# Optimization experiments

Measured on AMD Instinct MI355X. Metric: run time of the kernel, lower is better.

The kernel has to match this reference:

```python
import jax, jax.numpy as jnp
import numpy as np

N = 10000
E = 160000
NT = 4      # num_types
NB = 8      # bessel basis size
U = 32      # env_embed_multiplicity
R_MAX = 6.0
AVG_NEIGH = 16.0
POLY_P = 6.0


def _mlp(x, Ws):
    # nequip ScalarMLPFunction: no biases, forward-normalized weights, SiLU between layers
    n = len(Ws)
    for i, W in enumerate(Ws):
        x = x @ (W * (1.0 / jnp.sqrt(jnp.float32(W.shape[0]))))
        if i < n - 1:
            x = jax.nn.silu(x)
    return x


def _poly_cutoff(r, rc, p=POLY_P):
    x = r / rc
    out = (1.0 - ((p + 1.0) * (p + 2.0) / 2.0) * x ** p
           + p * (p + 2.0) * x ** (p + 1.0)
           - (p * (p + 1.0) / 2.0) * x ** (p + 2.0))
    return out * (x < 1.0)


def _weighted_channels(edge_attr, w):
    # MakeWeightedChannels: per-edge, per-channel weight for each irrep block
    # edge_attr: [E,4] = (0e | 1o), w: [E,U,2] -> out [E,U,4]
    wd = jnp.concatenate([w[:, :, 0:1], jnp.repeat(w[:, :, 1:2], 3, axis=-1)], axis=-1)
    return edge_attr[:, None, :] * wd


def _forward(edge_index, node_attrs, edge_attr, edge_embed, edge_length,
             W2b0, W2b1, W2b2, Wenv0, Wlat0, Wlat1, Wenv1, Wfin0, Wfin1,
             Wlin_s, Wlin_v, resnet_params):
    n_nodes = node_attrs.shape[0]
    n_edges = edge_attr.shape[0]
    center, neigh = edge_index[0], edge_index[1]
    cut = _poly_cutoff(edge_length, R_MAX)[:, None]           # [E,1], same per-layer cutoff
    env_norm = 1.0 / jnp.sqrt(AVG_NEIGH)
    sqrt3 = jnp.sqrt(3.0)
    c = jnp.exp(resnet_params)                                 # resnet update coefficients

    # ---- two-body latent (layer 0 latent)
    lat_in = jnp.concatenate([node_attrs[center], node_attrs[neigh], edge_embed], axis=-1)
    latents = _mlp(lat_in, [W2b0, W2b1, W2b2]) * cut           # [E,512]
    norm2 = c[0] ** 2
    latents = latents * (c[0] / jnp.sqrt(norm2))

    # env-embed MLP layer 0: feature weights + env weights
    w0 = _mlp(latents, [Wenv0])                                # [E,4U]
    w_feat = w0[:, :2 * U].reshape(n_edges, U, 2)
    w_env = w0[:, 2 * U:].reshape(n_edges, U, 2)
    features = _weighted_channels(edge_attr, w_feat)           # [E,U,4]

    def env_embed_edges(w_env):
        env_w = _weighted_channels(edge_attr, w_env)           # [E,U,4]
        env = jax.ops.segment_sum(env_w, center, num_segments=n_nodes) * env_norm
        return env[center]                                     # [E,U,4]

    # ---- layer 0 TP ('uuu', e3nn component norm): (0e+1o) x (0e+1o) -> [0e,0e,1o,1o]
    env_e = env_embed_edges(w_env)
    t0 = features[:, :, 0] * env_e[:, :, 0]
    t1 = jnp.sum(features[:, :, 1:] * env_e[:, :, 1:], axis=-1) / sqrt3
    v0 = features[:, :, 0:1] * env_e[:, :, 1:]
    v1 = features[:, :, 1:] * env_e[:, :, 0:1]
    scalars = jnp.concatenate([t0, t1], axis=-1)               # [E,2U]
    # e3nn Linear mixing full_out_irreps back to (0e+1o) x U
    alpha = 1.0 / jnp.sqrt(2.0 * U)
    y_s = (scalars @ Wlin_s) * alpha                           # [E,U]
    x_v = jnp.concatenate([v0, v1], axis=1)                    # [E,2U,3]
    y_v = jnp.einsum('ekd,ko->eod', x_v, Wlin_v) * alpha       # [E,U,3]
    features = jnp.concatenate([y_s[..., None], y_v], axis=-1)

    # latent resnet update
    new_lat = _mlp(jnp.concatenate([latents, scalars], axis=-1), [Wlat0, Wlat1]) * cut
    latents = (jnp.sqrt(norm2) * latents + c[1] * new_lat) / jnp.sqrt(norm2 + c[1] ** 2)
    norm2 = norm2 + c[1] ** 2

    w_env = _mlp(latents, [Wenv1]).reshape(n_edges, U, 2)

    # ---- layer 1 TP (last layer): only scalar outputs [0e,0e]
    env_e = env_embed_edges(w_env)
    t0 = features[:, :, 0] * env_e[:, :, 0]
    t1 = jnp.sum(features[:, :, 1:] * env_e[:, :, 1:], axis=-1) / sqrt3
    scalars = jnp.concatenate([t0, t1], axis=-1)               # [E,2U]
    # (the last-layer Linear output features are never used downstream -> skipped)

    # ---- final latent
    new_lat = _mlp(jnp.concatenate([latents, scalars], axis=-1), [Wfin0, Wfin1]) * cut
    latents = (jnp.sqrt(norm2) * latents + c[2] * new_lat) / jnp.sqrt(norm2 + c[2] ** 2)
    return latents                                             # [E,512] edge features


def setup_inputs() -> dict:
    key = jax.random.key(0)
    ks = jax.random.split(key, 20)
    edge_index = jax.random.randint(ks[0], (2, E), 0, N)
    node_types = jax.random.randint(ks[1], (N,), 0, NT)
    node_attrs = jax.nn.one_hot(node_types, NT, dtype=jnp.float32)
    edge_length = jax.random.uniform(ks[2], (E,), minval=0.5, maxval=R_MAX)
    vec = jax.random.normal(ks[3], (E, 3), dtype=jnp.float32)
    unit = vec / jnp.linalg.norm(vec, axis=-1, keepdims=True)
    # component-normalized real spherical harmonics: l=0 -> 1, l=1 -> sqrt(3)*unit
    edge_attr = jnp.concatenate([jnp.ones((E, 1), jnp.float32), jnp.sqrt(3.0) * unit], axis=-1)
    nb = jnp.arange(1, NB + 1, dtype=jnp.float32)
    edge_embed = (jnp.sqrt(2.0 / R_MAX)
                  * jnp.sin(nb[None, :] * jnp.pi * edge_length[:, None] / R_MAX)
                  / edge_length[:, None])
    w = lambda k, shp: jax.random.normal(k, shp, dtype=jnp.float32)
    return {
        'edge_index': edge_index, 'node_attrs': node_attrs, 'edge_attr': edge_attr,
        'edge_embed': edge_embed, 'edge_length': edge_length,
        'W2b0': w(ks[4], (2 * NT + NB, 128)), 'W2b1': w(ks[5], (128, 256)), 'W2b2': w(ks[6], (256, 512)),
        'Wenv0': w(ks[7], (512, 4 * U)),
        'Wlat0': w(ks[8], (512 + 2 * U, 512)), 'Wlat1': w(ks[9], (512, 512)),
        'Wenv1': w(ks[10], (512, 2 * U)),
        'Wfin0': w(ks[11], (512 + 2 * U, 512)), 'Wfin1': w(ks[12], (512, 512)),
        'Wlin_s': w(ks[13], (2 * U, U)), 'Wlin_v': w(ks[14], (2 * U, U)),
        'resnet_params': jnp.zeros((3,), jnp.float32),
    }


def reference(edge_index, node_attrs, edge_attr, edge_embed, edge_length,
              W2b0, W2b1, W2b2, Wenv0, Wlat0, Wlat1, Wenv1, Wfin0, Wfin1,
              Wlin_s, Wlin_v, resnet_params):
    return _forward(edge_index, node_attrs, edge_attr, edge_embed, edge_length,
                    W2b0, W2b1, W2b2, Wenv0, Wlat0, Wlat1, Wenv1, Wfin0, Wfin1,
                    Wlin_s, Wlin_v, resnet_params)
```

## Files before the change

kernel.cpp:

```cpp
#include <hip/hip_runtime.h>
#include <math.h>

#define E_EDGES 160000
#define N_NODES 10000

typedef __attribute__((ext_vector_type(8))) __bf16 bf16x8;
typedef __attribute__((ext_vector_type(4))) float f32x4;
typedef __attribute__((ext_vector_type(4))) unsigned int u32x4;

__device__ __forceinline__ unsigned short f2bf(float x) {
    unsigned u = __float_as_uint(x);
    u += 0x7fff + ((u >> 16) & 1);
    return (unsigned short)(u >> 16);
}
__device__ __forceinline__ float bf2f(unsigned short h) {
    return __uint_as_float(((unsigned)h) << 16);
}
__device__ __forceinline__ float siluf(float v) {
    return v / (1.0f + __expf(-v));
}
__device__ __forceinline__ void gload16(const unsigned short* g, unsigned short* l) {
    __builtin_amdgcn_global_load_lds(
        (const __attribute__((address_space(1))) void*)g,
        (__attribute__((address_space(3))) void*)l, 16, 0, 0);
}

__global__ __launch_bounds__(256)
void prep_kernel(const int* __restrict__ ei, const float* __restrict__ na,
                 const float* __restrict__ embed, const float* __restrict__ elen,
                 float* __restrict__ cut, unsigned short* __restrict__ A16b,
                 int* __restrict__ deg)
{
    int e = blockIdx.x * blockDim.x + threadIdx.x;
    if (e >= E_EDGES) return;
    float r  = elen[e];
    float x  = r * (1.0f / 6.0f);
    float x2 = x * x;
    float x6 = x2 * x2 * x2;
    float c = 1.0f - 28.0f * x6 + 48.0f * x6 * x - 21.0f * x6 * x2;
    cut[e] = (x < 1.0f) ? c : 0.0f;
    int ctr = ei[e];
    int ngh = ei[E_EDGES + e];
    atomicAdd(&deg[ctr], 1);
    float4 ac = *(const float4*)(na + (size_t)ctr * 4);
    float4 an = *(const float4*)(na + (size_t)ngh * 4);
    float4 b0 = *(const float4*)(embed + (size_t)e * 8);
    float4 b1 = *(const float4*)(embed + (size_t)e * 8 + 4);
    unsigned short* o = A16b + (size_t)e * 32;
    o[0]  = f2bf(ac.x); o[1]  = f2bf(ac.y); o[2]  = f2bf(ac.z); o[3]  = f2bf(ac.w);
    o[4]  = f2bf(an.x); o[5]  = f2bf(an.y); o[6]  = f2bf(an.z); o[7]  = f2bf(an.w);
    o[8]  = f2bf(b0.x); o[9]  = f2bf(b0.y); o[10] = f2bf(b0.z); o[11] = f2bf(b0.w);
    o[12] = f2bf(b1.x); o[13] = f2bf(b1.y); o[14] = f2bf(b1.z); o[15] = f2bf(b1.w);
    #pragma unroll
    for (int i = 16; i < 32; ++i) o[i] = 0;
}

__global__ __launch_bounds__(256)
void wtrans_all(const float* __restrict__ w0, const float* __restrict__ w1,
                const float* __restrict__ w2, const float* __restrict__ w3,
                const float* __restrict__ w4, const float* __restrict__ w5,
                const float* __restrict__ w6, const float* __restrict__ w7,
                const float* __restrict__ w8, unsigned short* __restrict__ wbuf)
{
    int blk = blockIdx.x;
    const float* W; int K, N, Kpad, Npad; size_t dbase; int lstart; float sc;
    const float s16  = 0.25f;
    const float s128 = 0.088388347648318447f;
    const float s256 = 0.0625f;
    const float s512 = 0.044194173824159223f;
    const float s576 = 0.041666666666666664f;
    if      (blk <   16) { W=w0; K=16;  N=128; Kpad=32;  Npad=128; dbase=0;       lstart=0;    sc=s16;  }
    else if (blk <  144) { W=w1; K=128; N=256; Kpad=128; Npad=256; dbase=4096;    lstart=16;   sc=s128; }
    else if (blk <  656) { W=w2; K=256; N=512; Kpad=256; Npad=512; dbase=36864;   lstart=144;  sc=s256; }
    else if (blk <  912) { W=w3; K=512; N=128; Kpad=512; Npad=128; dbase=167936;  lstart=656;  sc=s512; }
    else if (blk < 2064) { W=w4; K=576; N=512; Kpad=576; Npad=512; dbase=233472;  lstart=912;  sc=s576; }
    else if (blk < 3088) { W=w5; K=512; N=512; Kpad=512; Npad=512; dbase=528384;  lstart=2064; sc=s512; }
    else if (blk < 3344) { W=w6; K=512; N=64;  Kpad=512; Npad=128; dbase=790528;  lstart=3088; sc=s512; }
    else if (blk < 4496) { W=w7; K=576; N=512; Kpad=576; Npad=512; dbase=856064;  lstart=3344; sc=s576; }
    else                 { W=w8; K=512; N=512; Kpad=512; Npad=512; dbase=1150976; lstart=4496; sc=s512; }
    int local = (blk - lstart) * 256 + threadIdx.x;
    int n = local % Npad, k = local / Npad;
    if (k >= Kpad) return;
    float v = (k < K && n < N) ? W[(size_t)k * N + n] * sc : 0.0f;
    wbuf[dbase + (size_t)n * Kpad + k] = f2bf(v);
}

__global__ __launch_bounds__(1024)
void scan_kernel(const int* __restrict__ deg, int* __restrict__ offs)
{
    __shared__ int part[1024];
    int t = threadIdx.x;
    int base = t * 10;
    int loc[10];
    int s = 0;
    #pragma unroll
    for (int i = 0; i < 10; ++i) {
        int idx = base + i;
        int d = (idx < N_NODES) ? deg[idx] : 0;
        loc[i] = s; s += d;
    }
    part[t] = s;
    __syncthreads();
    for (int o = 1; o < 1024; o <<= 1) {
        int v = (t >= o) ? part[t - o] : 0;
        __syncthreads();
        part[t] += v;
        __syncthreads();
    }
    int excl = (t > 0) ? part[t - 1] : 0;
    #pragma unroll
    for (int i = 0; i < 10; ++i) {
        int idx = base + i;
        if (idx < N_NODES) offs[idx] = excl + loc[i];
    }
    if (t == 1023) offs[N_NODES] = part[1023];
}

__global__ __launch_bounds__(256)
void fill_kernel(const int* __restrict__ ei, const int* __restrict__ offs,
                 int* __restrict__ cnt, int* __restrict__ elist)
{
    int e = blockIdx.x * blockDim.x + threadIdx.x;
    if (e >= E_EDGES) return;
    int c = ei[e];
    int pos = offs[c] + atomicAdd(&cnt[c], 1);
    elist[pos] = e;
}

__global__ __launch_bounds__(256)
void sortseg_kernel(const int* __restrict__ offs, int* __restrict__ elist)
{
    int node = blockIdx.x * 4 + (threadIdx.x >> 6);
    int l = threadIdx.x & 63;
    if (node >= N_NODES) return;
    int b = offs[node], en = offs[node + 1];
    int deg = en - b;
    if (deg <= 1) return;
    if (deg <= 64) {
        int v = (l < deg) ? elist[b + l] : 0x7fffffff;
        #pragma unroll
        for (int k = 2; k <= 64; k <<= 1) {
            #pragma unroll
            for (int j = k >> 1; j > 0; j >>= 1) {
                int o = __shfl_xor(v, j);
                bool dirUp = ((l & k) == 0);
                bool lower = ((l & j) == 0);
                int mn = v < o ? v : o;
                int mx = v < o ? o : v;
                v = (dirUp == lower) ? mn : mx;
            }
        }
        if (l < deg) elist[b + l] = v;
    } else if (l == 0) {
        for (int i = b + 1; i < en; ++i) {
            int v = elist[i];
            int j = i - 1;
            while (j >= b && elist[j] > v) { elist[j + 1] = elist[j]; --j; }
            elist[j + 1] = v;
        }
    }
}

__global__ __launch_bounds__(256)
void envgather_kernel(const unsigned short* __restrict__ Wb, int wstride, int woff,
                      const float* __restrict__ ea, const int* __restrict__ offs,
                      const int* __restrict__ elist, float* __restrict__ env)
{
    int n = blockIdx.x * 2 + (threadIdx.x >> 7);
    int t = threadIdx.x & 127;
    if (n >= N_NODES) return;
    int u = t >> 2, comp = t & 3;
    int widx = woff + u * 2 + (comp ? 1 : 0);
    int beg = offs[n], end = offs[n + 1];
    float acc = 0.0f;
    for (int i = beg; i < end; ++i) {
        int e = elist[i];
        float w = bf2f(Wb[(size_t)e * wstride + widx]);
        float a = ea[(size_t)e * 4 + comp];
        acc += a * w;
    }
    env[(size_t)n * 128 + t] = acc * 0.25f;
}

__global__ __launch_bounds__(512)
void mlp2b(const unsigned short* __restrict__ A16b,
           const unsigned short* __restrict__ W0t,
           const unsigned short* __restrict__ W1t,
           const unsigned short* __restrict__ W2t,
           const unsigned short* __restrict__ Wet,
           const float* __restrict__ cut,
           unsigned short* __restrict__ Lb,
           unsigned short* __restrict__ R1b)
{
    __shared__ __align__(16) unsigned short SA[64 * 32];
    __shared__ __align__(16) unsigned short RG[64 * 512];
    unsigned short* H1 = RG;
    unsigned short* H2 = RG + 8192;
    const int tid  = threadIdx.x;
    const int lane = tid & 63;
    const int wid  = tid >> 6;
    const int l15  = lane & 15;
    const int l4r  = lane >> 2;
    const int lk8  = (lane >> 4) << 3;
    const int sk8  = (((lane & 3) ^ ((lane >> 3) & 3)) << 3);
    const int rk8  = ((((lane >> 4) ^ ((l15 >> 1) & 3)) & 3) << 3);
    const int bm   = blockIdx.x * 64;
    const int hrow4 = (lane >> 4) << 2;

    if (wid < 4) {
        int row = (wid << 4) + l4r;
        gload16(A16b + (size_t)(bm + row) * 32 + sk8, &SA[wid << 9]);
    }
    asm volatile("s_waitcnt vmcnt(0)" ::: "memory");
    __builtin_amdgcn_s_barrier();
    __builtin_amdgcn_sched_barrier(0);

    {
        int hc = wid * 16 + l15;
        bf16x8 wf = __builtin_bit_cast(bf16x8, *(const u32x4*)(W0t + (size_t)hc * 32 + lk8));
        #pragma unroll
        for (int mi = 0; mi < 4; ++mi) {
            bf16x8 af = __builtin_bit_cast(bf16x8, *(const u32x4*)&SA[(mi * 16 + l15) * 32 + rk8]);
            f32x4 a = {};
            a = __builtin_amdgcn_mfma_f32_16x16x32_bf16(af, wf, a, 0, 0, 0);
            #pragma unroll
            for (int rr = 0; rr < 4; ++rr) {
                int er = mi * 16 + hrow4 + rr;
                H1[er * 128 + (((hc >> 3) ^ (er & 7)) << 3) + (hc & 7)] = f2bf(siluf(a[rr]));
            }
        }
    }
    asm volatile("s_waitcnt lgkmcnt(0)" ::: "memory");
    __builtin_amdgcn_s_barrier();
    __builtin_amdgcn_sched_barrier(0);

    {
        f32x4 acc[4][2] = {};
        #pragma unroll
        for (int kt = 0; kt < 4; ++kt) {
            bf16x8 hf[4], wf[2];
            #pragma unroll
            for (int fa = 0; fa < 4; ++fa) {
                int er = fa * 16 + l15;
                int slotp = (kt * 4 + (lane >> 4)) ^ (er & 7);
                hf[fa] = __builtin_bit_cast(bf16x8, *(const u32x4*)&H1[er * 128 + slotp * 8]);
            }
            #pragma unroll
            for (int fb = 0; fb < 2; ++fb) {
                int hc = wid * 32 + fb * 16 + l15;
                wf[fb] = __builtin_bit_cast(bf16x8, *(const u32x4*)(W1t + (size_t)hc * 128 + kt * 32 + lk8));
            }
            #pragma unroll
            for (int fa = 0; fa < 4; ++fa)
                #pragma unroll
                for (int fb = 0; fb < 2; ++fb)
                    acc[fa][fb] = __builtin_amdgcn_mfma_f32_16x16x32_bf16(hf[fa], wf[fb], acc[fa][fb], 0, 0, 0);
        }
        asm volatile("s_waitcnt lgkmcnt(0)" ::: "memory");
        __builtin_amdgcn_s_barrier();
        #pragma unroll
        for (int fa = 0; fa < 4; ++fa)
            #pragma unroll
            for (int fb = 0; fb < 2; ++fb)
                #pragma unroll
                for (int rr = 0; rr < 4; ++rr) {
                    int er = fa * 16 + hrow4 + rr;
                    int hc = wid * 32 + fb * 16 + l15;
                    H2[er * 256 + (((hc >> 3) ^ (er & 7)) << 3) + (hc & 7)] = f2bf(siluf(acc[fa][fb][rr]));
                }
    }
    asm volatile("s_waitcnt lgkmcnt(0)" ::: "memory");
    __builtin_amdgcn_s_barrier();
    __builtin_amdgcn_sched_barrier(0);

    f32x4 acc[4][4] = {};
    #pragma unroll 1
    for (int kt = 0; kt < 8; ++kt) {
        bf16x8 hf[4], wf[4];
        #pragma unroll
        for (int fa = 0; fa < 4; ++fa) {
            int er = fa * 16 + l15;
            int slotp = (kt * 4 + (lane >> 4)) ^ (er & 7);
            hf[fa] = __builtin_bit_cast(bf16x8, *(const u32x4*)&H2[er * 256 + slotp * 8]);
        }
        #pragma unroll
        for (int fb = 0; fb < 4; ++fb) {
            int oc = wid * 64 + fb * 16 + l15;
            wf[fb] = __builtin_bit_cast(bf16x8, *(const u32x4*)(W2t + (size_t)oc * 256 + kt * 32 + lk8));
        }
        __builtin_amdgcn_s_setprio(1);
        #pragma unroll
        for (int fa = 0; fa < 4; ++fa)
            #pragma unroll
            for (int fb = 0; fb < 4; ++fb)
                acc[fa][fb] = __builtin_amdgcn_mfma_f32_16x16x32_bf16(hf[fa], wf[fb], acc[fa][fb], 0, 0, 0);
        __builtin_amdgcn_s_setprio(0);
    }
    asm volatile("s_waitcnt lgkmcnt(0)" ::: "memory");
    __builtin_amdgcn_s_barrier();
    __builtin_amdgcn_sched_barrier(0);

    #pragma unroll
    for (int fa = 0; fa < 4; ++fa) {
        int rbase = bm + fa * 16 + hrow4;
        #pragma unroll
        for (int fb = 0; fb < 4; ++fb) {
            int col = wid * 64 + fb * 16 + l15;
            #pragma unroll
            for (int rr = 0; rr < 4; ++rr) {
                int row = rbase + rr;
                int er  = fa * 16 + hrow4 + rr;
                float v = acc[fa][fb][rr] * cut[row];
                unsigned short b = f2bf(v);
                Lb[(size_t)row * 512 + col] = b;
                RG[er * 512 + (((col >> 3) ^ (er & 7)) << 3) + (col & 7)] = b;
            }
        }
    }
    asm volatile("s_waitcnt lgkmcnt(0)" ::: "memory");
    __builtin_amdgcn_s_barrier();
    __builtin_amdgcn_sched_barrier(0);

    {
        f32x4 acce[4] = {};
        int oc = wid * 16 + l15;
        #pragma unroll 1
        for (int kt = 0; kt < 16; ++kt) {
            bf16x8 wfe = __builtin_bit_cast(bf16x8, *(const u32x4*)(Wet + (size_t)oc * 512 + kt * 32 + lk8));
            #pragma unroll
            for (int fa = 0; fa < 4; ++fa) {
                int er = fa * 16 + l15;
                int slotp = (kt * 4 + (lane >> 4)) ^ (er & 7);
                bf16x8 afe = __builtin_bit_cast(bf16x8, *(const u32x4*)&RG[er * 512 + slotp * 8]);
                acce[fa] = __builtin_amdgcn_mfma_f32_16x16x32_bf16(afe, wfe, acce[fa], 0, 0, 0);
            }
        }
        #pragma unroll
        for (int fa = 0; fa < 4; ++fa) {
            int rbase = bm + fa * 16 + hrow4;
            #pragma unroll
            for (int rr = 0; rr < 4; ++rr)
                R1b[(size_t)(rbase + rr) * 128 + wid * 16 + l15] = f2bf(acce[fa][rr]);
        }
    }
}

template<int EPIL2, bool ENV>
__global__ __launch_bounds__(512)
void fused_mlp(const unsigned short* __restrict__ A1,
               const unsigned short* __restrict__ A2,
               const unsigned short* __restrict__ W1t,
               const unsigned short* __restrict__ W2t,
               const unsigned short* __restrict__ Wet,
               float* __restrict__ Cf, unsigned short* __restrict__ Cb,
               unsigned short* __restrict__ Weo,
               const float* __restrict__ cut, const float* __restrict__ rp)
{
    __shared__ __align__(16) unsigned short Hl[128 * 512];
    __shared__ __align__(16) unsigned short SA[3][128 * 32];
    const int tid  = threadIdx.x;
    const int lane = tid & 63;
    const int wid  = tid >> 6;
    const int l15  = lane & 15;
    const int l4r  = lane >> 2;
    const int lk8  = (lane >> 4) << 3;
    const int sk8  = (((lane & 3) ^ ((lane >> 3) & 3)) << 3);
    const int rk8  = ((((lane >> 4) ^ ((l15 >> 1) & 3)) & 3) << 3);
    const int bm   = blockIdx.x * 128;
    const int col0 = wid * 64;
    const int hrow4 = (lane >> 4) << 2;

    auto stage = [&](int t, int b) {
        int k0 = t << 5;
        int row = (wid << 4) + l4r;
        const unsigned short* gp;
        if (k0 < 512) gp = A1 + (size_t)(bm + row) * 512 + k0 + sk8;
        else          gp = A2 + (size_t)(bm + row) * 64 + (k0 - 512) + sk8;
        gload16(gp, &SA[b][wid << 9]);
    };

    f32x4 acc1[8][4] = {};
    stage(0, 0);
    stage(1, 1);

    for (int t = 0; t < 18; ++t) {
        __builtin_amdgcn_sched_barrier(0);
        if (t < 17) asm volatile("s_waitcnt vmcnt(1)" ::: "memory");
        else        asm volatile("s_waitcnt vmcnt(0)" ::: "memory");
        __builtin_amdgcn_s_barrier();
        __builtin_amdgcn_sched_barrier(0);

        const unsigned short* As = &SA[t % 3][0];
        int k0 = t << 5;
        bf16x8 af[8], wf[4];
        #pragma unroll
        for (int mi = 0; mi < 8; ++mi)
            af[mi] = __builtin_bit_cast(bf16x8, *(const u32x4*)&As[(mi * 16 + l15) * 32 + rk8]);
        #pragma unroll
        for (int ni = 0; ni < 4; ++ni) {
            int hc = col0 + ni * 16 + l15;
            wf[ni] = __builtin_bit_cast(bf16x8, *(const u32x4*)(W1t + (size_t)hc * 576 + k0 + lk8));
        }
        __builtin_amdgcn_sched_barrier(0);
        if (t + 2 < 18) stage(t + 2, (t + 2) % 3);
        __builtin_amdgcn_sched_barrier(0);
        asm volatile("s_waitcnt lgkmcnt(0)" ::: "memory");
        __builtin_amdgcn_sched_barrier(0);

        __builtin_amdgcn_s_setprio(1);
        #pragma unroll
        for (int mi = 0; mi < 8; ++mi)
            #pragma unroll
            for (int ni = 0; ni < 4; ++ni)
                acc1[mi][ni] = __builtin_amdgcn_mfma_f32_16x16x32_bf16(af[mi], wf[ni], acc1[mi][ni], 0, 0, 0);
        __builtin_amdgcn_s_setprio(0);
    }

    #pragma unroll
    for (int mi = 0; mi < 8; ++mi)
        #pragma unroll
        for (int ni = 0; ni < 4; ++ni)
            #pragma unroll
            for (int rr = 0; rr < 4; ++rr) {
                int er = mi * 16 + hrow4 + rr;
                int hc = col0 + ni * 16 + l15;
                Hl[er * 512 + (((hc >> 3) ^ (er & 7)) << 3) + (hc & 7)] = f2bf(siluf(acc1[mi][ni][rr]));
            }
    asm volatile("s_waitcnt lgkmcnt(0)" ::: "memory");
    __builtin_amdgcn_s_barrier();
    __builtin_amdgcn_sched_barrier(0);

    f32x4 acc2[8][4] = {};
    #pragma unroll 1
    for (int kt = 0; kt < 16; ++kt) {
        bf16x8 hf[8], w2f[4];
        #pragma unroll
        for (int fa = 0; fa < 8; ++fa) {
            int er = fa * 16 + l15;
            int slotp = (kt * 4 + (lane >> 4)) ^ (er & 7);
            hf[fa] = __builtin_bit_cast(bf16x8, *(const u32x4*)&Hl[er * 512 + slotp * 8]);
        }
        #pragma unroll
        for (int fb = 0; fb < 4; ++fb) {
            int oc = col0 + fb * 16 + l15;
            w2f[fb] = __builtin_bit_cast(bf16x8, *(const u32x4*)(W2t + (size_t)oc * 512 + kt * 32 + lk8));
        }
        __builtin_amdgcn_s_setprio(1);
        #pragma unroll
        for (int fa = 0; fa < 8; ++fa)
            #pragma unroll
            for (int fb = 0; fb < 4; ++fb)
                acc2[fa][fb] = __builtin_amdgcn_mfma_f32_16x16x32_bf16(hf[fa], w2f[fb], acc2[fa][fb], 0, 0, 0);
        __builtin_amdgcn_s_setprio(0);
    }

    if constexpr (ENV) {
        asm volatile("s_waitcnt lgkmcnt(0)" ::: "memory");
        __builtin_amdgcn_s_barrier();
        __builtin_amdgcn_sched_barrier(0);
    }

    float c0 = __expf(rp[0]), c1 = __expf(rp[1]), c2 = __expf(rp[2]);
    #pragma unroll
    for (int fa = 0; fa < 8; ++fa) {
        int rbase = bm + fa * 16 + hrow4;
        #pragma unroll
        for (int fb = 0; fb < 4; ++fb) {
            int col = col0 + fb * 16 + l15;
            #pragma unroll
            for (int rr = 0; rr < 4; ++rr) {
                int row = rbase + rr;
                int er  = fa * 16 + hrow4 + rr;
                float v = acc2[fa][fb][rr];
                size_t off2 = (size_t)row * 512 + col;
                if (EPIL2 == 3) {
                    float old = bf2f(Cb[off2]);
                    v = (c0 * old + c1 * v * cut[row]) * rsqrtf(c0 * c0 + c1 * c1);
                    unsigned short b = f2bf(v);
                    Cb[off2] = b;
                    if constexpr (ENV)
                        Hl[er * 512 + (((col >> 3) ^ (er & 7)) << 3) + (col & 7)] = b;
                } else {
                    float old = bf2f(Cb[off2]);
                    float n2 = c0 * c0 + c1 * c1;
                    v = (sqrtf(n2) * old + c2 * v * cut[row]) * rsqrtf(n2 + c2 * c2);
                    Cf[off2] = v;
                }
            }
        }
    }

    if constexpr (ENV) {
        asm volatile("s_waitcnt lgkmcnt(0)" ::: "memory");
        __builtin_amdgcn_s_barrier();
        __builtin_amdgcn_sched_barrier(0);
        f32x4 acce[4] = {};
        int er = wid * 16 + l15;
        #pragma unroll 1
        for (int kt = 0; kt < 16; ++kt) {
            int slotp = (kt * 4 + (lane >> 4)) ^ (er & 7);
            bf16x8 afe = __builtin_bit_cast(bf16x8, *(const u32x4*)&Hl[er * 512 + slotp * 8]);
            #pragma unroll
            for (int fb = 0; fb < 4; ++fb) {
                int oc = fb * 16 + l15;
                bf16x8 wfe = __builtin_bit_cast(bf16x8, *(const u32x4*)(Wet + (size_t)oc * 512 + kt * 32 + lk8));
                acce[fb] = __builtin_amdgcn_mfma_f32_16x16x32_bf16(afe, wfe, acce[fb], 0, 0, 0);
            }
        }
        #pragma unroll
        for (int fb = 0; fb < 4; ++fb) {
            int col = fb * 16 + l15;
            #pragma unroll
            for (int rr = 0; rr < 4; ++rr) {
                int row = bm + wid * 16 + hrow4 + rr;
                Weo[(size_t)row * 64 + col] = f2bf(acce[fb][rr]);
            }
        }
    }
}

__global__ __launch_bounds__(256)
void tp0_kernel(const unsigned short* __restrict__ W0b, const float* __restrict__ ea,
                const float* __restrict__ env, const int* __restrict__ ei,
                const float* __restrict__ Ws, const float* __restrict__ Wv,
                unsigned short* __restrict__ scalb, unsigned short* __restrict__ feat2b)
{
    __shared__ float sc[8][64];
    __shared__ float xv[8][64][3];
    __shared__ float Wsl[2048];
    __shared__ float Wvl[2048];
    int tid = threadIdx.x;
    const float alpha = 0.125f;
    #pragma unroll
    for (int i = 0; i < 8; ++i) {
        Wsl[tid + i * 256] = Ws[tid + i * 256] * alpha;
        Wvl[tid + i * 256] = Wv[tid + i * 256] * alpha;
    }
    int le = tid >> 5;
    int u  = tid & 31;
    int e  = blockIdx.x * 8 + le;
    int c  = ei[e];
    float4 a = *(const float4*)(ea + (size_t)e * 4);
    const float* ep = env + (size_t)c * 128 + u * 4;
    float e0 = ep[0], e1 = ep[1], e2 = ep[2], e3 = ep[3];
    float wf0 = bf2f(W0b[(size_t)e * 128 + u * 2]);
    float wf1 = bf2f(W0b[(size_t)e * 128 + u * 2 + 1]);
    float f0 = a.x * wf0;
    float f1 = a.y * wf1, f2 = a.z * wf1, f3 = a.w * wf1;
    const float rs3 = 0.57735026918962576f;
    float t0 = f0 * e0;
    float t1 = (f1 * e1 + f2 * e2 + f3 * e3) * rs3;
    scalb[(size_t)e * 64 + u]      = f2bf(t0);
    scalb[(size_t)e * 64 + 32 + u] = f2bf(t1);
    sc[le][u]      = t0;
    sc[le][32 + u] = t1;
    xv[le][u][0] = f0 * e1; xv[le][u][1] = f0 * e2; xv[le][u][2] = f0 * e3;
    xv[le][32 + u][0] = f1 * e0; xv[le][32 + u][1] = f2 * e0; xv[le][32 + u][2] = f3 * e0;
    __syncthreads();
    float ys = 0.0f, yv0 = 0.0f, yv1 = 0.0f, yv2 = 0.0f;
    #pragma unroll 8
    for (int k = 0; k < 64; ++k) {
        float ws = Wsl[k * 32 + u];
        float wv = Wvl[k * 32 + u];
        ys  = fmaf(sc[le][k], ws, ys);
        yv0 = fmaf(xv[le][k][0], wv, yv0);
        yv1 = fmaf(xv[le][k][1], wv, yv1);
        yv2 = fmaf(xv[le][k][2], wv, yv2);
    }
    ushort4 ov;
    ov.x = f2bf(ys);
    ov.y = f2bf(yv0);
    ov.z = f2bf(yv1);
    ov.w = f2bf(yv2);
    *(ushort4*)(feat2b + (size_t)e * 128 + u * 4) = ov;
}

__global__ __launch_bounds__(256)
void tp1_kernel(const unsigned short* __restrict__ feat2b, const float* __restrict__ env,
                const int* __restrict__ ei, unsigned short* __restrict__ scalb)
{
    int idx = blockIdx.x * blockDim.x + threadIdx.x;
    if (idx >= E_EDGES * 32) return;
    int e = idx >> 5, u = idx & 31;
    int c = ei[e];
    const float* ep = env + (size_t)c * 128 + u * 4;
    ushort4 f4 = *(const ushort4*)(feat2b + (size_t)e * 128 + u * 4);
    float fx = bf2f(f4.x), fy = bf2f(f4.y), fz = bf2f(f4.z), fw = bf2f(f4.w);
    const float rs3 = 0.57735026918962576f;
    float t0 = fx * ep[0];
    float t1 = (fy * ep[1] + fz * ep[2] + fw * ep[3]) * rs3;
    scalb[(size_t)e * 64 + u]      = f2bf(t0);
    scalb[(size_t)e * 64 + 32 + u] = f2bf(t1);
}

extern "C" void kernel_launch(void* const* d_in, const int* in_sizes, int n_in,
                              void* d_out, int out_size, void* d_ws, size_t ws_size,
                              hipStream_t stream)
{
    const int*   ei     = (const int*)d_in[0];
    const float* na     = (const float*)d_in[1];
    const float* ea     = (const float*)d_in[2];
    const float* embed  = (const float*)d_in[3];
    const float* elen   = (const float*)d_in[4];
    const float* W2b0   = (const float*)d_in[5];
    const float* W2b1   = (const float*)d_in[6];
    const float* W2b2   = (const float*)d_in[7];
    const float* Wenv0  = (const float*)d_in[8];
    const float* Wlat0  = (const float*)d_in[9];
    const float* Wlat1  = (const float*)d_in[10];
    const float* Wenv1  = (const float*)d_in[11];
    const float* Wfin0  = (const float*)d_in[12];
    const float* Wfin1  = (const float*)d_in[13];
    const float* Wlin_s = (const float*)d_in[14];
    const float* Wlin_v = (const float*)d_in[15];
    const float* rp     = (const float*)d_in[16];

    float* L = (float*)d_out;
    const size_t E = E_EDGES;

    char* ws = (char*)d_ws;
    size_t off = 0;
    auto alloc = [&](size_t b) { void* p = ws + off; off += (b + 255) & ~(size_t)255; return p; };
    float*          cutb   = (float*)alloc(E * 4);
    unsigned short* wbuf   = (unsigned short*)alloc((size_t)1413120 * 2);
    float*          envb   = (float*)alloc((size_t)N_NODES * 128 * 4);
    unsigned short* scalb  = (unsigned short*)alloc(E * 64 * 2);
    unsigned short* feat2b = (unsigned short*)alloc(E * 128 * 2);
    unsigned short* Lb     = (unsigned short*)alloc(E * 512 * 2);
    int*            degcnt = (int*)alloc((size_t)2 * N_NODES * 4);
    int*            offs   = (int*)alloc((N_NODES + 1) * 4);
    int*            elist  = (int*)alloc(E * 4);
    unsigned short* A16b   = (unsigned short*)alloc(E * 32 * 2);
    unsigned short* R1b    = (unsigned short*)alloc(E * 128 * 2);
    unsigned short* WE1b   = (unsigned short*)alloc(E * 64 * 2);
    int* deg = degcnt;
    int* cnt = degcnt + N_NODES;

    unsigned short* W2b0t  = wbuf;
    unsigned short* W2b1t  = wbuf + 4096;
    unsigned short* W2b2t  = wbuf + 36864;
    unsigned short* Wenv0t = wbuf + 167936;
    unsigned short* Wlat0t = wbuf + 233472;
    unsigned short* Wlat1t = wbuf + 528384;
    unsigned short* Wenv1t = wbuf + 790528;
    unsigned short* Wfin0t = wbuf + 856064;
    unsigned short* Wfin1t = wbuf + 1150976;
    wtrans_all<<<5520, 256, 0, stream>>>(W2b0, W2b1, W2b2, Wenv0, Wlat0, Wlat1,
                                         Wenv1, Wfin0, Wfin1, wbuf);

    hipMemsetAsync(degcnt, 0, (size_t)2 * N_NODES * 4, stream);
    prep_kernel<<<E_EDGES / 256, 256, 0, stream>>>(ei, na, embed, elen, cutb, A16b, deg);
    scan_kernel<<<1, 1024, 0, stream>>>(deg, offs);
    fill_kernel<<<E_EDGES / 256, 256, 0, stream>>>(ei, offs, cnt, elist);
    sortseg_kernel<<<N_NODES / 4, 256, 0, stream>>>(offs, elist);

    mlp2b<<<2500, 512, 0, stream>>>(A16b, W2b0t, W2b1t, W2b2t, Wenv0t, cutb, Lb, R1b);

    envgather_kernel<<<N_NODES / 2, 256, 0, stream>>>(R1b, 128, 64, ea, offs, elist, envb);
    tp0_kernel<<<E_EDGES / 8, 256, 0, stream>>>(R1b, ea, envb, ei, Wlin_s, Wlin_v, scalb, feat2b);

    fused_mlp<3, true><<<1250, 512, 0, stream>>>(Lb, scalb, Wlat0t, Wlat1t, Wenv1t,
                                                 nullptr, Lb, WE1b, cutb, rp);

    envgather_kernel<<<N_NODES / 2, 256, 0, stream>>>(WE1b, 64, 0, ea, offs, elist, envb);
    tp1_kernel<<<E_EDGES * 32 / 256, 256, 0, stream>>>(feat2b, envb, ei, scalb);

    fused_mlp<4, false><<<1250, 512, 0, stream>>>(Lb, scalb, Wfin0t, Wfin1t, nullptr,
                                                  L, Lb, nullptr, cutb, rp);
}
```

Measured before the change: 1.196 ms.

## Stage first-GEMM weight tiles into LDS via async loads in fused MLP kernels

The first GEMM in both fused MLP kernels used to read W1 fragments straight from global memory every k-step. It now streams the 512x32 weight tile into the otherwise idle Hl buffer with async global-to-LDS loads, triple-buffered next to the A tiles, and reads fragments from LDS. The template is split into two concrete kernels, waits are adjusted to vmcnt(5), and a barrier is added before Hl is reused for the hidden activations. This is meant to hide global weight-load latency behind the MFMA work, at the cost of more LDS traffic and more outstanding loads per wave.

```diff
diff --git a/kernel.cpp b/kernel.cpp
--- a/kernel.cpp
+++ b/kernel.cpp
@@ -345,16 +345,15 @@
     }
 }
 
-template<int EPIL2, bool ENV>
 __global__ __launch_bounds__(512)
-void fused_mlp(const unsigned short* __restrict__ A1,
-               const unsigned short* __restrict__ A2,
-               const unsigned short* __restrict__ W1t,
-               const unsigned short* __restrict__ W2t,
-               const unsigned short* __restrict__ Wet,
-               float* __restrict__ Cf, unsigned short* __restrict__ Cb,
-               unsigned short* __restrict__ Weo,
-               const float* __restrict__ cut, const float* __restrict__ rp)
+void fused_mlp3env(const unsigned short* __restrict__ A1,
+                   const unsigned short* __restrict__ A2,
+                   const unsigned short* __restrict__ W1t,
+                   const unsigned short* __restrict__ W2t,
+                   const unsigned short* __restrict__ Wet,
+                   unsigned short* __restrict__ Cb,
+                   unsigned short* __restrict__ Weo,
+                   const float* __restrict__ cut, const float* __restrict__ rp)
 {
     __shared__ __align__(16) unsigned short Hl[128 * 512];
     __shared__ __align__(16) unsigned short SA[3][128 * 32];
@@ -370,7 +369,7 @@
     const int col0 = wid * 64;
     const int hrow4 = (lane >> 4) << 2;
 
-    auto stage = [&](int t, int b) {
+    auto stageA = [&](int t, int b) {
         int k0 = t << 5;
         int row = (wid << 4) + l4r;
         const unsigned short* gp;
@@ -378,34 +377,37 @@
         else          gp = A2 + (size_t)(bm + row) * 64 + (k0 - 512) + sk8;
         gload16(gp, &SA[b][wid << 9]);
     };
+    auto stageW = [&](int t, int b) {
+        int k0 = t << 5;
+        #pragma unroll
+        for (int i = 0; i < 4; ++i) {
+            int ch  = (wid << 2) + i;
+            int row = (ch << 4) + l4r;
+            gload16(W1t + (size_t)row * 576 + k0 + sk8, &Hl[b * 16384 + (ch << 9)]);
+        }
+    };
 
     f32x4 acc1[8][4] = {};
-    stage(0, 0);
-    stage(1, 1);
+    stageA(0, 0); stageW(0, 0);
+    stageA(1, 1); stageW(1, 1);
 
     for (int t = 0; t < 18; ++t) {
-        __builtin_amdgcn_sched_barrier(0);
-        if (t < 17) asm volatile("s_waitcnt vmcnt(1)" ::: "memory");
+        if (t < 17) asm volatile("s_waitcnt vmcnt(5)" ::: "memory");
         else        asm volatile("s_waitcnt vmcnt(0)" ::: "memory");
         __builtin_amdgcn_s_barrier();
         __builtin_amdgcn_sched_barrier(0);
 
+        if (t + 2 < 18) { stageA(t + 2, (t + 2) % 3); stageW(t + 2, (t + 2) % 3); }
+
         const unsigned short* As = &SA[t % 3][0];
-        int k0 = t << 5;
+        const unsigned short* Ws = &Hl[(t % 3) * 16384];
         bf16x8 af[8], wf[4];
         #pragma unroll
         for (int mi = 0; mi < 8; ++mi)
             af[mi] = __builtin_bit_cast(bf16x8, *(const u32x4*)&As[(mi * 16 + l15) * 32 + rk8]);
         #pragma unroll
-        for (int ni = 0; ni < 4; ++ni) {
-            int hc = col0 + ni * 16 + l15;
-            wf[ni] = __builtin_bit_cast(bf16x8, *(const u32x4*)(W1t + (size_t)hc * 576 + k0 + lk8));
-        }
-        __builtin_amdgcn_sched_barrier(0);
-        if (t + 2 < 18) stage(t + 2, (t + 2) % 3);
-        __builtin_amdgcn_sched_barrier(0);
-        asm volatile("s_waitcnt lgkmcnt(0)" ::: "memory");
-        __builtin_amdgcn_sched_barrier(0);
+        for (int ni = 0; ni < 4; ++ni)
+            wf[ni] = __builtin_bit_cast(bf16x8, *(const u32x4*)&Ws[(col0 + ni * 16 + l15) * 32 + rk8]);
 
         __builtin_amdgcn_s_setprio(1);
         #pragma unroll
@@ -415,6 +417,9 @@
                 acc1[mi][ni] = __builtin_amdgcn_mfma_f32_16x16x32_bf16(af[mi], wf[ni], acc1[mi][ni], 0, 0, 0);
         __builtin_amdgcn_s_setprio(0);
     }
+    asm volatile("s_waitcnt lgkmcnt(0)" ::: "memory");
+    __builtin_amdgcn_s_barrier();
+    __builtin_amdgcn_sched_barrier(0);
 
     #pragma unroll
     for (int mi = 0; mi < 8; ++mi)
@@ -454,13 +459,11 @@
         __builtin_amdgcn_s_setprio(0);
     }
 
-    if constexpr (ENV) {
-        asm volatile("s_waitcnt lgkmcnt(0)" ::: "memory");
-        __builtin_amdgcn_s_barrier();
-        __builtin_amdgcn_sched_barrier(0);
-    }
-
-    float c0 = __expf(rp[0]), c1 = __expf(rp[1]), c2 = __expf(rp[2]);
+    asm volatile("s_waitcnt lgkmcnt(0)" ::: "memory");
+    __builtin_amdgcn_s_barrier();
+    __builtin_amdgcn_sched_barrier(0);
+
+    float c0 = __expf(rp[0]), c1 = __expf(rp[1]);
     #pragma unroll
     for (int fa = 0; fa < 8; ++fa) {
         int rbase = bm + fa * 16 + hrow4;
@@ -473,27 +476,19 @@
                 int er  = fa * 16 + hrow4 + rr;
                 float v = acc2[fa][fb][rr];
                 size_t off2 = (size_t)row * 512 + col;
-                if (EPIL2 == 3) {
-                    float old = bf2f(Cb[off2]);
-                    v = (c0 * old + c1 * v * cut[row]) * rsqrtf(c0 * c0 + c1 * c1);
-                    unsigned short b = f2bf(v);
-                    Cb[off2] = b;
-                    if constexpr (ENV)
-                        Hl[er * 512 + (((col >> 3) ^ (er & 7)) << 3) + (col & 7)] = b;
-                } else {
-                    float old = bf2f(Cb[off2]);
-                    float n2 = c0 * c0 + c1 * c1;
-                    v = (sqrtf(n2) * old + c2 * v * cut[row]) * rsqrtf(n2 + c2 * c2);
-                    Cf[off2] = v;
-                }
-            }
-        }
-    }
-
-    if constexpr (ENV) {
-        asm volatile("s_waitcnt lgkmcnt(0)" ::: "memory");
-        __builtin_amdgcn_s_barrier();
-        __builtin_amdgcn_sched_barrier(0);
+                float old = bf2f(Cb[off2]);
+                v = (c0 * old + c1 * v * cut[row]) * rsqrtf(c0 * c0 + c1 * c1);
+                unsigned short b = f2bf(v);
+                Cb[off2] = b;
+                Hl[er * 512 + (((col >> 3) ^ (er & 7)) << 3) + (col & 7)] = b;
+            }
+        }
+    }
+    asm volatile("s_waitcnt lgkmcnt(0)" ::: "memory");
+    __builtin_amdgcn_s_barrier();
+    __builtin_amdgcn_sched_barrier(0);
+
+    {
         f32x4 acce[4] = {};
         int er = wid * 16 + l15;
         #pragma unroll 1
@@ -514,6 +509,139 @@
             for (int rr = 0; rr < 4; ++rr) {
                 int row = bm + wid * 16 + hrow4 + rr;
                 Weo[(size_t)row * 64 + col] = f2bf(acce[fb][rr]);
+            }
+        }
+    }
+}
+
+__global__ __launch_bounds__(512)
+void fused_mlp4(const unsigned short* __restrict__ A1,
+                const unsigned short* __restrict__ A2,
+                const unsigned short* __restrict__ W1t,
+                const unsigned short* __restrict__ W2t,
+                float* __restrict__ Cf, const unsigned short* __restrict__ Cb,
+                const float* __restrict__ cut, const float* __restrict__ rp)
+{
+    __shared__ __align__(16) unsigned short Hl[128 * 512];
+    __shared__ __align__(16) unsigned short SA[3][128 * 32];
+    const int tid  = threadIdx.x;
+    const int lane = tid & 63;
+    const int wid  = tid >> 6;
+    const int l15  = lane & 15;
+    const int l4r  = lane >> 2;
+    const int lk8  = (lane >> 4) << 3;
+    const int sk8  = (((lane & 3) ^ ((lane >> 3) & 3)) << 3);
+    const int rk8  = ((((lane >> 4) ^ ((l15 >> 1) & 3)) & 3) << 3);
+    const int bm   = blockIdx.x * 128;
+    const int col0 = wid * 64;
+    const int hrow4 = (lane >> 4) << 2;
+
+    auto stageA = [&](int t, int b) {
+        int k0 = t << 5;
+        int row = (wid << 4) + l4r;
+        const unsigned short* gp;
+        if (k0 < 512) gp = A1 + (size_t)(bm + row) * 512 + k0 + sk8;
+        else          gp = A2 + (size_t)(bm + row) * 64 + (k0 - 512) + sk8;
+        gload16(gp, &SA[b][wid << 9]);
+    };
+    auto stageW = [&](int t, int b) {
+        int k0 = t << 5;
+        #pragma unroll
+        for (int i = 0; i < 4; ++i) {
+            int ch  = (wid << 2) + i;
+            int row = (ch << 4) + l4r;
+            gload16(W1t + (size_t)row * 576 + k0 + sk8, &Hl[b * 16384 + (ch << 9)]);
+        }
+    };
+
+    f32x4 acc1[8][4] = {};
+    stageA(0, 0); stageW(0, 0);
+    stageA(1, 1); stageW(1, 1);
+
+    for (int t = 0; t < 18; ++t) {
+        if (t < 17) asm volatile("s_waitcnt vmcnt(5)" ::: "memory");
+        else        asm volatile("s_waitcnt vmcnt(0)" ::: "memory");
+        __builtin_amdgcn_s_barrier();
+        __builtin_amdgcn_sched_barrier(0);
+
+        if (t + 2 < 18) { stageA(t + 2, (t + 2) % 3); stageW(t + 2, (t + 2) % 3); }
+
+        const unsigned short* As = &SA[t % 3][0];
+        const unsigned short* Ws = &Hl[(t % 3) * 16384];
+        bf16x8 af[8], wf[4];
+        #pragma unroll
+        for (int mi = 0; mi < 8; ++mi)
+            af[mi] = __builtin_bit_cast(bf16x8, *(const u32x4*)&As[(mi * 16 + l15) * 32 + rk8]);
+        #pragma unroll
+        for (int ni = 0; ni < 4; ++ni)
+            wf[ni] = __builtin_bit_cast(bf16x8, *(const u32x4*)&Ws[(col0 + ni * 16 + l15) * 32 + rk8]);
+
+        __builtin_amdgcn_s_setprio(1);
+        #pragma unroll
+        for (int mi = 0; mi < 8; ++mi)
+            #pragma unroll
+            for (int ni = 0; ni < 4; ++ni)
+                acc1[mi][ni] = __builtin_amdgcn_mfma_f32_16x16x32_bf16(af[mi], wf[ni], acc1[mi][ni], 0, 0, 0);
+        __builtin_amdgcn_s_setprio(0);
+    }
+    asm volatile("s_waitcnt lgkmcnt(0)" ::: "memory");
+    __builtin_amdgcn_s_barrier();
+    __builtin_amdgcn_sched_barrier(0);
+
+    #pragma unroll
+    for (int mi = 0; mi < 8; ++mi)
+        #pragma unroll
+        for (int ni = 0; ni < 4; ++ni)
+            #pragma unroll
+            for (int rr = 0; rr < 4; ++rr) {
+                int er = mi * 16 + hrow4 + rr;
+                int hc = col0 + ni * 16 + l15;
+                Hl[er * 512 + (((hc >> 3) ^ (er & 7)) << 3) + (hc & 7)] = f2bf(siluf(acc1[mi][ni][rr]));
+            }
+    asm volatile("s_waitcnt lgkmcnt(0)" ::: "memory");
+    __builtin_amdgcn_s_barrier();
+    __builtin_amdgcn_sched_barrier(0);
+
+    f32x4 acc2[8][4] = {};
+    #pragma unroll 1
+    for (int kt = 0; kt < 16; ++kt) {
+        bf16x8 hf[8], w2f[4];
+        #pragma unroll
+        for (int fa = 0; fa < 8; ++fa) {
+            int er = fa * 16 + l15;
+            int slotp = (kt * 4 + (lane >> 4)) ^ (er & 7);
+            hf[fa] = __builtin_bit_cast(bf16x8, *(const u32x4*)&Hl[er * 512 + slotp * 8]);
+        }
+        #pragma unroll
+        for (int fb = 0; fb < 4; ++fb) {
+            int oc = col0 + fb * 16 + l15;
+            w2f[fb] = __builtin_bit_cast(bf16x8, *(const u32x4*)(W2t + (size_t)oc * 512 + kt * 32 + lk8));
+        }
+        __builtin_amdgcn_s_setprio(1);
+        #pragma unroll
+        for (int fa = 0; fa < 8; ++fa)
+            #pragma unroll
+            for (int fb = 0; fb < 4; ++fb)
+                acc2[fa][fb] = __builtin_amdgcn_mfma_f32_16x16x32_bf16(hf[fa], w2f[fb], acc2[fa][fb], 0, 0, 0);
+        __builtin_amdgcn_s_setprio(0);
+    }
+
+    float c0 = __expf(rp[0]), c1 = __expf(rp[1]), c2 = __expf(rp[2]);
+    #pragma unroll
+    for (int fa = 0; fa < 8; ++fa) {
+        int rbase = bm + fa * 16 + hrow4;
+        #pragma unroll
+        for (int fb = 0; fb < 4; ++fb) {
+            int col = col0 + fb * 16 + l15;
+            #pragma unroll
+            for (int rr = 0; rr < 4; ++rr) {
+                int row = rbase + rr;
+                float v = acc2[fa][fb][rr];
+                size_t off2 = (size_t)row * 512 + col;
+                float old = bf2f(Cb[off2]);
+                float n2 = c0 * c0 + c1 * c1;
+                v = (sqrtf(n2) * old + c2 * v * cut[row]) * rsqrtf(n2 + c2 * c2);
+                Cf[off2] = v;
             }
         }
     }
@@ -659,12 +787,11 @@
     envgather_kernel<<<N_NODES / 2, 256, 0, stream>>>(R1b, 128, 64, ea, offs, elist, envb);
     tp0_kernel<<<E_EDGES / 8, 256, 0, stream>>>(R1b, ea, envb, ei, Wlin_s, Wlin_v, scalb, feat2b);
 
-    fused_mlp<3, true><<<1250, 512, 0, stream>>>(Lb, scalb, Wlat0t, Wlat1t, Wenv1t,
-                                                 nullptr, Lb, WE1b, cutb, rp);
+    fused_mlp3env<<<1250, 512, 0, stream>>>(Lb, scalb, Wlat0t, Wlat1t, Wenv1t,
+                                            Lb, WE1b, cutb, rp);
 
     envgather_kernel<<<N_NODES / 2, 256, 0, stream>>>(WE1b, 64, 0, ea, offs, elist, envb);
     tp1_kernel<<<E_EDGES * 32 / 256, 256, 0, stream>>>(feat2b, envb, ei, scalb);
 
-    fused_mlp<4, false><<<1250, 512, 0, stream>>>(Lb, scalb, Wfin0t, Wfin1t, nullptr,
-                                                  L, Lb, nullptr, cutb, rp);
-}
+    fused_mlp4<<<1250, 512, 0, stream>>>(Lb, scalb, Wfin0t, Wfin1t, L, Lb, cutb, rp);
+}
```

Result: no change. 1.203 ms (+0.7%).
